# Kernel optimization log

Measured on AMD Instinct MI355X. Metric: run time of the kernel, lower is better.

Reference implementation:

```python
import jax, jax.numpy as jnp
import numpy as np
import math

B, H, S, DK = 4, 16, 2048, 64

def setup_inputs() -> dict:
    key = jax.random.key(0)
    kq, kk, kv, km = jax.random.split(key, 4)
    Q = jax.random.normal(kq, (B, H, S, DK), dtype=jnp.float32)
    K = jax.random.normal(kk, (B, H, S, DK), dtype=jnp.float32)
    V = jax.random.normal(kv, (B, H, S, DK), dtype=jnp.float32)
    # boolean mask [B, Sq, Sk]; True positions are masked out (set to -1e9)
    mask = jax.random.randint(km, (B, S, S), 0, 2).astype(jnp.bool_)
    return {"Q": Q, "K": K, "V": V, "mask": mask}

def reference(Q, K, V, mask):
    d_k = Q.shape[-1]
    # [B,H,Sq,Sk] scores
    scores = jnp.einsum('bhqd,bhkd->bhqk', Q, K) / math.sqrt(d_k)
    # mask [B,Sq,Sk] broadcasts over head dim (torch code repeats over heads)
    scores = jnp.where(mask[:, None, :, :], jnp.float32(-1e9), scores)
    attn = jax.nn.softmax(scores, axis=-1)
    out = jnp.einsum('bhqk,bhkd->bhqd', attn, V)
    return (out, attn)
```

## Files before the change

### kernel.cpp

```cpp
#include <hip/hip_runtime.h>
#include <cstdint>
#include <cstddef>

#define S_LEN 2048
#define DKD   64
#define BQ    64
#define BK    128
#define NKT   16
#define BDIM  256

typedef float f32x4 __attribute__((ext_vector_type(4)));
typedef short s16x8 __attribute__((ext_vector_type(8)));
typedef short s16x4 __attribute__((ext_vector_type(4)));
typedef unsigned short u16t;
typedef unsigned long long u64t;

#define KS_OFF    0
#define KT_BYTES  (BK * DKD * 2)
#define VT_OFF    16384
#define VT_BYTES  (DKD * BK * 2)
#define PS_OFF    32768
#define PS_STRIDE 264
#define SMEM_SZ   (PS_OFF + BQ * PS_STRIDE)

__device__ __forceinline__ u16t f2bf(float f) {
  unsigned u = __builtin_bit_cast(unsigned, f);
  return (u16t)((u + 0x7FFFu + ((u >> 16) & 1u)) >> 16);
}
__device__ __forceinline__ float bf_lo(unsigned u) {
  return __builtin_bit_cast(float, u << 16);
}
__device__ __forceinline__ float bf_hi(unsigned u) {
  return __builtin_bit_cast(float, u & 0xFFFF0000u);
}

__device__ __forceinline__ void gl_lds16(const void* g, void* l) {
  typedef __attribute__((address_space(1))) void gvoid;
  typedef __attribute__((address_space(3))) void lvoid;
  __builtin_amdgcn_global_load_lds((gvoid*)(void*)g, (lvoid*)l, 16, 0, 0);
}

#define BAR_VM(N) do { asm volatile("s_waitcnt vmcnt(" #N ")\n\ts_barrier" ::: "memory"); \
                       __builtin_amdgcn_sched_barrier(0); } while (0)
#define BAR_LGKM() do { asm volatile("s_waitcnt lgkmcnt(0)\n\ts_barrier" ::: "memory"); \
                        __builtin_amdgcn_sched_barrier(0); } while (0)

__global__ __launch_bounds__(256)
void prologue(const unsigned char* __restrict__ Mg, const float* __restrict__ Kg,
              const float* __restrict__ Vg, u64t* __restrict__ bits,
              u16t* __restrict__ Kws, u16t* __restrict__ Vws) {
  __shared__ float scr[BK][DKD + 1];
  __shared__ int mflag_s;
  const int tid = threadIdx.x;
  const int bid = blockIdx.x;

  if (bid < 1024) {
    int f = 0;
    for (int i = tid; i < 4096; i += 256) if ((i & 3) && Mg[i]) f = 1;
    if (tid == 0) mflag_s = 0;
    __syncthreads();
    if (f) mflag_s = 1;
    __syncthreads();
    const int mstride = mflag_s ? 1 : 4;

    const int row = bid * 8 + (tid >> 5);
    const int wd  = tid & 31;
    const size_t kbase = (size_t)row * S_LEN + (size_t)wd * 64;
    u64t word = 0;
    if (mstride == 1) {
      const u64t* p = (const u64t*)(Mg + kbase);
      #pragma unroll
      for (int i = 0; i < 8; ++i) {
        u64t x = p[i];
        u64t nz = x | (x >> 4); nz |= nz >> 2; nz |= nz >> 1;
        nz &= 0x0101010101010101ull;
        word |= ((nz * 0x0102040810204080ull) >> 56) << (8 * i);
      }
    } else {
      const unsigned* p = (const unsigned*)Mg + kbase;
      #pragma unroll
      for (int i = 0; i < 64; ++i) word |= (u64t)(p[i] ? 1u : 0u) << i;
    }
    bits[(size_t)row * 32 + wd] = word;
  } else if (bid < 2048) {
    const int kb = bid - 1024;
    const float* src = Kg + (size_t)kb * (BK * DKD);
    u16t* dst = Kws + (size_t)kb * (BK * DKD);
    #pragma unroll
    for (int i = 0; i < 4; ++i) {
      int c = tid + 256 * i;
      int row = c >> 3, y = c & 7;
      int oc = y ^ (row & 7);
      const float4* s4 = (const float4*)(src + row * DKD + 8 * oc);
      float4 a = s4[0], b = s4[1];
      s16x8 h = { (short)f2bf(a.x), (short)f2bf(a.y), (short)f2bf(a.z), (short)f2bf(a.w),
                  (short)f2bf(b.x), (short)f2bf(b.y), (short)f2bf(b.z), (short)f2bf(b.w) };
      *(s16x8*)(dst + row * DKD + 8 * y) = h;
    }
  } else {
    const int vb = bid - 2048;
    const float4* src = (const float4*)(Vg + (size_t)vb * (BK * DKD));
    #pragma unroll
    for (int i = 0; i < 8; ++i) {
      int c = tid + 256 * i;
      float4 v = src[c];
      int k = c >> 4, d0 = (c & 15) * 4;
      scr[k][d0] = v.x; scr[k][d0 + 1] = v.y; scr[k][d0 + 2] = v.z; scr[k][d0 + 3] = v.w;
    }
    __syncthreads();
    u16t* dst = Vws + (size_t)vb * (DKD * BK);
    #pragma unroll
    for (int i = 0; i < 8; ++i) {
      int c = tid + 256 * i;
      int dv = c >> 5, y = c & 31;
      int k0 = 4 * (y ^ (dv & 7));
      ushort4 h = make_ushort4(f2bf(scr[k0][dv]), f2bf(scr[k0 + 1][dv]),
                               f2bf(scr[k0 + 2][dv]), f2bf(scr[k0 + 3][dv]));
      *(ushort4*)(dst + dv * BK + 4 * y) = h;
    }
  }
}

__global__ __launch_bounds__(256)
void attn_ws(const float* __restrict__ Qg, const u16t* __restrict__ Kws,
             const u16t* __restrict__ Vws, const u64t* __restrict__ bits,
             float* __restrict__ outg, float* __restrict__ attng) {
  __shared__ char smem[SMEM_SZ];
  const int tid = threadIdx.x;
  const int p = blockIdx.x;
  const int qb = (p >> 3) & 31;
  const int bh = (p & 7) + 8 * (p >> 8);
  const int b  = bh >> 4;
  const int lane = tid & 63, wv = tid >> 6;
  const int cl = lane & 15, g = lane >> 4;
  const int q0 = qb * BQ + 16 * wv + 4 * g;
  const int swzK = (cl & 7) << 4;
  const int swzV = (cl & 7) << 3;

  const char* Kbh = (const char*)Kws + (size_t)bh * NKT * KT_BYTES;
  const char* Vbh = (const char*)Vws + (size_t)bh * NKT * VT_BYTES;

  float* oRow[4]; const u64t* bitRow[4];
  #pragma unroll
  for (int r = 0; r < 4; ++r) {
    oRow[r] = outg + (size_t)(bh * S_LEN + q0 + r) * DKD + cl;
    bitRow[r] = bits + (size_t)(b * S_LEN + q0 + r) * 32;
  }
  float* attnQ = attng + ((size_t)bh * S_LEN + (size_t)qb * BQ) * S_LEN;

  s16x8 aq0, aq1;
  {
    const float* qrow = Qg + ((size_t)bh * S_LEN + qb * BQ + 16 * wv + cl) * DKD;
    float x[8], y[8];
    *(float4*)(x)     = *(const float4*)(qrow + 8 * g);
    *(float4*)(x + 4) = *(const float4*)(qrow + 8 * g + 4);
    *(float4*)(y)     = *(const float4*)(qrow + 32 + 8 * g);
    *(float4*)(y + 4) = *(const float4*)(qrow + 32 + 8 * g + 4);
    #pragma unroll
    for (int j = 0; j < 8; ++j) { aq0[j] = (short)f2bf(x[j]); aq1[j] = (short)f2bf(y[j]); }
  }

  auto stageK = [&](int kt, int off) {
    const char* src = Kbh + (size_t)kt * KT_BYTES + wv * 4096 + lane * 16;
    #pragma unroll
    for (int t = 0; t < 4; ++t)
      gl_lds16(src + t * 1024, (void*)(smem + off + wv * 4096 + t * 1024));
  };
  auto stageV = [&](int kt) {
    const char* src = Vbh + (size_t)kt * VT_BYTES + wv * 4096 + lane * 16;
    #pragma unroll
    for (int t = 0; t < 4; ++t)
      gl_lds16(src + t * 1024, (void*)(smem + VT_OFF + wv * 4096 + t * 1024));
  };

  float lsum[4] = {0.f, 0.f, 0.f, 0.f};
  stageK(0, KS_OFF);
  for (int kt = 0; kt < NKT; ++kt) {
    const int cur = (kt & 1) ? VT_OFF : KS_OFF;
    if (kt + 1 < NKT) {
      stageK(kt + 1, (kt & 1) ? KS_OFF : VT_OFF);
      BAR_VM(4);
    } else {
      BAR_VM(0);
    }
    f32x4 accs[8];
    #pragma unroll
    for (int s = 0; s < 8; ++s) {
      const char* rb = smem + cur + (16 * s + cl) * 128;
      s16x8 b0 = *(const s16x8*)(rb + ((16 * g) ^ swzK));
      s16x8 b1 = *(const s16x8*)(rb + ((64 + 16 * g) ^ swzK));
      f32x4 acc = {0.f, 0.f, 0.f, 0.f};
      acc = __builtin_amdgcn_mfma_f32_16x16x32_bf16(aq0, b0, acc, 0, 0, 0);
      acc = __builtin_amdgcn_mfma_f32_16x16x32_bf16(aq1, b1, acc, 0, 0, 0);
      accs[s] = acc;
    }
    u64t bw0[4], bw1[4];
    #pragma unroll
    for (int r = 0; r < 4; ++r) { bw0[r] = bitRow[r][2 * kt]; bw1[r] = bitRow[r][2 * kt + 1]; }
    #pragma unroll
    for (int r = 0; r < 4; ++r) {
      float sum = 0.f;
      #pragma unroll
      for (int s = 0; s < 8; ++s) {
        bool mk = (((s < 4) ? bw0[r] : bw1[r]) >> ((16 * s + cl) & 63)) & 1ull;
        float e = __expf(accs[s][r] * 0.125f);
        sum += mk ? 0.f : e;
      }
      lsum[r] += sum;
    }
    BAR_LGKM();
  }
  float rinv[4];
  #pragma unroll
  for (int r = 0; r < 4; ++r) {
    float l = lsum[r];
    #pragma unroll
    for (int d = 1; d < 16; d <<= 1) l += __shfl_xor(l, d);
    rinv[r] = 1.f / l;
  }

  f32x4 accpv[4];
  #pragma unroll
  for (int db = 0; db < 4; ++db) accpv[db] = (f32x4){0.f, 0.f, 0.f, 0.f};

  stageK(0, KS_OFF);
  stageV(0);
  for (int kt = 0; kt < NKT; ++kt) {
    __syncthreads();
    u64t bw0[4], bw1[4];
    #pragma unroll
    for (int r = 0; r < 4; ++r) { bw0[r] = bitRow[r][2 * kt]; bw1[r] = bitRow[r][2 * kt + 1]; }

    #pragma unroll
    for (int ks = 0; ks < 4; ++ks) {
      f32x4 qa[2];
      #pragma unroll
      for (int sp = 0; sp < 2; ++sp) {
        int s = 2 * ks + sp;
        const char* rb = smem + KS_OFF + (16 * s + cl) * 128;
        s16x8 b0 = *(const s16x8*)(rb + ((16 * g) ^ swzK));
        s16x8 b1 = *(const s16x8*)(rb + ((64 + 16 * g) ^ swzK));
        f32x4 acc = {0.f, 0.f, 0.f, 0.f};
        acc = __builtin_amdgcn_mfma_f32_16x16x32_bf16(aq0, b0, acc, 0, 0, 0);
        acc = __builtin_amdgcn_mfma_f32_16x16x32_bf16(aq1, b1, acc, 0, 0, 0);
        qa[sp] = acc;
      }
      #pragma unroll
      for (int sp = 0; sp < 2; ++sp) {
        int s = 2 * ks + sp;
        #pragma unroll
        for (int r = 0; r < 4; ++r) {
          bool mk = (((s < 4) ? bw0[r] : bw1[r]) >> ((16 * s + cl) & 63)) & 1ull;
          float pv = mk ? 0.f : __expf(qa[sp][r] * 0.125f) * rinv[r];
          *(u16t*)(smem + PS_OFF + (16 * wv + 4 * g + r) * PS_STRIDE +
                   (32 * ks + 16 * sp + cl) * 2) = f2bf(pv);
        }
      }
      s16x4 p0 = *(const s16x4*)(smem + PS_OFF + (16 * wv + cl) * PS_STRIDE + (32 * ks + 4 * g) * 2);
      s16x4 p1 = *(const s16x4*)(smem + PS_OFF + (16 * wv + cl) * PS_STRIDE + (32 * ks + 16 + 4 * g) * 2);
      s16x8 pa = __builtin_shufflevector(p0, p1, 0, 1, 2, 3, 4, 5, 6, 7);
      #pragma unroll
      for (int db = 0; db < 4; ++db) {
        const char* vrow = smem + VT_OFF + (16 * db + cl) * 256;
        s16x4 v0 = *(const s16x4*)(vrow + ((64 * ks + 8 * g) ^ swzV));
        s16x4 v1 = *(const s16x4*)(vrow + ((64 * ks + 32 + 8 * g) ^ swzV));
        s16x8 vb = __builtin_shufflevector(v0, v1, 0, 1, 2, 3, 4, 5, 6, 7);
        accpv[db] = __builtin_amdgcn_mfma_f32_16x16x32_bf16(pa, vb, accpv[db], 0, 0, 0);
      }
    }
    __syncthreads();

    if (kt + 1 < NKT) { stageK(kt + 1, KS_OFF); stageV(kt + 1); }

    #pragma unroll
    for (int i = 0; i < 4; ++i) {
      int c = tid + 256 * i;
      int q = c >> 4, ch = c & 15;
      uint4 d = *(const uint4*)(smem + PS_OFF + q * PS_STRIDE + ch * 16);
      f32x4 lo = { bf_lo(d.x), bf_hi(d.x), bf_lo(d.y), bf_hi(d.y) };
      f32x4 hi = { bf_lo(d.z), bf_hi(d.z), bf_lo(d.w), bf_hi(d.w) };
      float* dst = attnQ + (size_t)q * S_LEN + kt * BK + ch * 8;
      __builtin_nontemporal_store(lo, (f32x4*)dst);
      __builtin_nontemporal_store(hi, (f32x4*)(dst + 4));
    }
  }

  #pragma unroll
  for (int db = 0; db < 4; ++db)
    #pragma unroll
    for (int r = 0; r < 4; ++r)
      oRow[r][16 * db] = accpv[db][r];
}

#define FB_KSTR 144
#define FB_VOFF (BK * FB_KSTR)
#define FB_VSTR 272
#define FB_POFF (FB_VOFF + DKD * FB_VSTR)
#define FB_SMEM (FB_POFF + BQ * FB_VSTR)

__global__ __launch_bounds__(256)
void attn_fb(const float* __restrict__ Qg, const float* __restrict__ Kg,
             const float* __restrict__ Vg, const unsigned char* __restrict__ Mg,
             float* __restrict__ outg, float* __restrict__ attng) {
  __shared__ char smem[FB_SMEM];
  __shared__ int mflag_s;
  const int tid = threadIdx.x;
  const int p = blockIdx.x;
  const int qb = (p >> 3) & 31;
  const int bh = (p & 7) + 8 * (p >> 8);
  const int b  = bh >> 4;

  int f = 0;
  for (int i = tid; i < 4096; i += BDIM) if ((i & 3) && Mg[i]) f = 1;
  if (tid == 0) mflag_s = 0;
  __syncthreads();
  if (f) mflag_s = 1;
  __syncthreads();
  const int mstride = mflag_s ? 1 : 4;

  const int lane = tid & 63, wv = tid >> 6;
  const int cl = lane & 15, g = lane >> 4;
  const int q0 = qb * BQ + 16 * wv + 4 * g;

  const float* Kbh = Kg + (size_t)bh * S_LEN * DKD;
  const float* Vbh = Vg + (size_t)bh * S_LEN * DKD;

  float* aRow[4]; float* oRow[4]; const unsigned char* mRow[4];
  #pragma unroll
  for (int r = 0; r < 4; ++r) {
    aRow[r] = attng + (size_t)(bh * S_LEN + q0 + r) * S_LEN + cl;
    oRow[r] = outg + (size_t)(bh * S_LEN + q0 + r) * DKD + cl;
    mRow[r] = Mg + ((size_t)(b * S_LEN + q0 + r) * S_LEN + cl) * (size_t)mstride;
  }

  s16x8 aq0, aq1;
  {
    const float* qrow = Qg + ((size_t)bh * S_LEN + qb * BQ + 16 * wv + cl) * DKD;
    float x[8], y[8];
    *(float4*)(x)     = *(const float4*)(qrow + 8 * g);
    *(float4*)(x + 4) = *(const float4*)(qrow + 8 * g + 4);
    *(float4*)(y)     = *(const float4*)(qrow + 32 + 8 * g);
    *(float4*)(y + 4) = *(const float4*)(qrow + 32 + 8 * g + 4);
    #pragma unroll
    for (int j = 0; j < 8; ++j) { aq0[j] = (short)f2bf(x[j]); aq1[j] = (short)f2bf(y[j]); }
  }

  float lsum[4] = {0.f, 0.f, 0.f, 0.f};
  for (int kt = 0; kt < NKT; ++kt) {
    const float4* ksrc = (const float4*)(Kbh + (size_t)kt * (BK * DKD));
    #pragma unroll
    for (int it = 0; it < 8; ++it) {
      int c = tid + BDIM * it;
      float4 v = ksrc[c];
      *(ushort4*)(smem + (c >> 4) * FB_KSTR + (c & 15) * 8) =
          make_ushort4(f2bf(v.x), f2bf(v.y), f2bf(v.z), f2bf(v.w));
    }
    __syncthreads();
    #pragma unroll
    for (int s = 0; s < 8; ++s) {
      s16x8 b0 = *(const s16x8*)(smem + (16 * s + cl) * FB_KSTR + 16 * g);
      s16x8 b1 = *(const s16x8*)(smem + (16 * s + cl) * FB_KSTR + 64 + 16 * g);
      f32x4 acc = {0.f, 0.f, 0.f, 0.f};
      acc = __builtin_amdgcn_mfma_f32_16x16x32_bf16(aq0, b0, acc, 0, 0, 0);
      acc = __builtin_amdgcn_mfma_f32_16x16x32_bf16(aq1, b1, acc, 0, 0, 0);
      #pragma unroll
      for (int r = 0; r < 4; ++r) {
        bool mk = mRow[r][(size_t)(kt * BK + 16 * s) * mstride] != 0;
        lsum[r] += mk ? 0.f : __expf(acc[r] * 0.125f);
      }
    }
    __syncthreads();
  }
  float rinv[4];
  #pragma unroll
  for (int r = 0; r < 4; ++r) {
    float l = lsum[r];
    #pragma unroll
    for (int d = 1; d < 16; d <<= 1) l += __shfl_xor(l, d);
    rinv[r] = 1.f / l;
  }

  f32x4 accpv[4];
  #pragma unroll
  for (int db = 0; db < 4; ++db) accpv[db] = (f32x4){0.f, 0.f, 0.f, 0.f};

  for (int kt = 0; kt < NKT; ++kt) {
    const float4* ksrc = (const float4*)(Kbh + (size_t)kt * (BK * DKD));
    #pragma unroll
    for (int it = 0; it < 8; ++it) {
      int c = tid + BDIM * it;
      float4 v = ksrc[c];
      *(ushort4*)(smem + (c >> 4) * FB_KSTR + (c & 15) * 8) =
          make_ushort4(f2bf(v.x), f2bf(v.y), f2bf(v.z), f2bf(v.w));
    }
    const float4* vsrc = (const float4*)(Vbh + (size_t)kt * (BK * DKD));
    #pragma unroll
    for (int it = 0; it < 8; ++it) {
      int c = tid + BDIM * it;
      float4 v = vsrc[c];
      int k = c >> 4, d0 = (c & 15) * 4;
      *(u16t*)(smem + FB_VOFF + (d0 + 0) * FB_VSTR + k * 2) = f2bf(v.x);
      *(u16t*)(smem + FB_VOFF + (d0 + 1) * FB_VSTR + k * 2) = f2bf(v.y);
      *(u16t*)(smem + FB_VOFF + (d0 + 2) * FB_VSTR + k * 2) = f2bf(v.z);
      *(u16t*)(smem + FB_VOFF + (d0 + 3) * FB_VSTR + k * 2) = f2bf(v.w);
    }
    __syncthreads();

    #pragma unroll
    for (int ks = 0; ks < 4; ++ks) {
      f32x4 qa[2];
      #pragma unroll
      for (int sp = 0; sp < 2; ++sp) {
        int s = 2 * ks + sp;
        s16x8 b0 = *(const s16x8*)(smem + (16 * s + cl) * FB_KSTR + 16 * g);
        s16x8 b1 = *(const s16x8*)(smem + (16 * s + cl) * FB_KSTR + 64 + 16 * g);
        f32x4 acc = {0.f, 0.f, 0.f, 0.f};
        acc = __builtin_amdgcn_mfma_f32_16x16x32_bf16(aq0, b0, acc, 0, 0, 0);
        acc = __builtin_amdgcn_mfma_f32_16x16x32_bf16(aq1, b1, acc, 0, 0, 0);
        qa[sp] = acc;
      }
      #pragma unroll
      for (int sp = 0; sp < 2; ++sp) {
        int s = 2 * ks + sp;
        #pragma unroll
        for (int r = 0; r < 4; ++r) {
          bool mk = mRow[r][(size_t)(kt * BK + 16 * s) * mstride] != 0;
          float pv = mk ? 0.f : __expf(qa[sp][r] * 0.125f) * rinv[r];
          __builtin_nontemporal_store(pv, aRow[r] + kt * BK + 16 * s);
          *(u16t*)(smem + FB_POFF + (16 * wv + 4 * g + r) * FB_VSTR +
                   (32 * ks + 16 * sp + cl) * 2) = f2bf(pv);
        }
      }
      s16x4 p0 = *(const s16x4*)(smem + FB_POFF + (16 * wv + cl) * FB_VSTR + (32 * ks + 4 * g) * 2);
      s16x4 p1 = *(const s16x4*)(smem + FB_POFF + (16 * wv + cl) * FB_VSTR + (32 * ks + 16 + 4 * g) * 2);
      s16x8 pa = __builtin_shufflevector(p0, p1, 0, 1, 2, 3, 4, 5, 6, 7);
      #pragma unroll
      for (int db = 0; db < 4; ++db) {
        s16x4 v0 = *(const s16x4*)(smem + FB_VOFF + (16 * db + cl) * FB_VSTR + (32 * ks + 4 * g) * 2);
        s16x4 v1 = *(const s16x4*)(smem + FB_VOFF + (16 * db + cl) * FB_VSTR + (32 * ks + 16 + 4 * g) * 2);
        s16x8 vb = __builtin_shufflevector(v0, v1, 0, 1, 2, 3, 4, 5, 6, 7);
        accpv[db] = __builtin_amdgcn_mfma_f32_16x16x32_bf16(pa, vb, accpv[db], 0, 0, 0);
      }
    }
    __syncthreads();
  }

  #pragma unroll
  for (int db = 0; db < 4; ++db)
    #pragma unroll
    for (int r = 0; r < 4; ++r)
      oRow[r][16 * db] = accpv[db][r];
}

extern "C" void kernel_launch(void* const* d_in, const int* in_sizes, int n_in,
                              void* d_out, int out_size, void* d_ws, size_t ws_size,
                              hipStream_t stream) {
  const float* Q = (const float*)d_in[0];
  const float* K = (const float*)d_in[1];
  const float* V = (const float*)d_in[2];
  const unsigned char* M = (const unsigned char*)d_in[3];
  float* out = (float*)d_out;
  float* attn = out + (size_t)4 * 16 * S_LEN * DKD;

  const size_t BITS_SZ = (size_t)4 * S_LEN * 32 * 8;
  const size_t KWS_SZ  = (size_t)64 * NKT * BK * DKD * 2;
  const size_t VWS_SZ  = (size_t)64 * NKT * DKD * BK * 2;
  if (ws_size >= BITS_SZ + KWS_SZ + VWS_SZ) {
    u64t* bits = (u64t*)d_ws;
    u16t* Kws = (u16t*)((char*)d_ws + BITS_SZ);
    u16t* Vws = (u16t*)((char*)d_ws + BITS_SZ + KWS_SZ);
    prologue<<<3072, 256, 0, stream>>>(M, K, V, bits, Kws, Vws);
    attn_ws<<<2048, BDIM, 0, stream>>>(Q, Kws, Vws, bits, out, attn);
  } else {
    attn_fb<<<2048, BDIM, 0, stream>>>(Q, K, V, M, out, attn);
  }
}
```

Before: 367.5 us.

## Transpose score MFMA so P stays in registers and simplify mask handling

The QK^T MFMA operands are swapped so each lane holds scores for a single query row. This lets the softmax denominator use one accumulator with two cross-lane shuffles, lets the mask be read as one 16-byte load per tile, and lets P be packed straight into the PV MFMA operand without an LDS write-then-read round trip. P is still written to LDS, with a new padded stride, for the attn output store. Full __syncthreads barriers are replaced with explicit waitcnt barriers that allow the attn stores to overlap the next tile's loads. The barrier choice (vmcnt(8) at the end of the loop) is fragile and could race if the count of outstanding memory ops changes.

```diff
diff --git a/kernel.cpp b/kernel.cpp
--- a/kernel.cpp
+++ b/kernel.cpp
@@ -12,6 +12,7 @@
 typedef float f32x4 __attribute__((ext_vector_type(4)));
 typedef short s16x8 __attribute__((ext_vector_type(8)));
 typedef short s16x4 __attribute__((ext_vector_type(4)));
+typedef unsigned int u32x4 __attribute__((ext_vector_type(4)));
 typedef unsigned short u16t;
 typedef unsigned long long u64t;
 
@@ -20,7 +21,7 @@
 #define VT_OFF    16384
 #define VT_BYTES  (DKD * BK * 2)
 #define PS_OFF    32768
-#define PS_STRIDE 264
+#define PS_STRIDE 280
 #define SMEM_SZ   (PS_OFF + BQ * PS_STRIDE)
 
 __device__ __forceinline__ u16t f2bf(float f) {
@@ -42,8 +43,10 @@
 
 #define BAR_VM(N) do { asm volatile("s_waitcnt vmcnt(" #N ")\n\ts_barrier" ::: "memory"); \
                        __builtin_amdgcn_sched_barrier(0); } while (0)
-#define BAR_LGKM() do { asm volatile("s_waitcnt lgkmcnt(0)\n\ts_barrier" ::: "memory"); \
-                        __builtin_amdgcn_sched_barrier(0); } while (0)
+#define BAR_LG()  do { asm volatile("s_waitcnt lgkmcnt(0)\n\ts_barrier" ::: "memory"); \
+                       __builtin_amdgcn_sched_barrier(0); } while (0)
+#define BAR_VM8() do { asm volatile("s_waitcnt vmcnt(8) lgkmcnt(0)\n\ts_barrier" ::: "memory"); \
+                       __builtin_amdgcn_sched_barrier(0); } while (0)
 
 __global__ __launch_bounds__(256)
 void prologue(const unsigned char* __restrict__ Mg, const float* __restrict__ Kg,
@@ -133,29 +136,28 @@
   const int b  = bh >> 4;
   const int lane = tid & 63, wv = tid >> 6;
   const int cl = lane & 15, g = lane >> 4;
-  const int q0 = qb * BQ + 16 * wv + 4 * g;
+  const int qrow = qb * BQ + 16 * wv + cl;
   const int swzK = (cl & 7) << 4;
   const int swzV = (cl & 7) << 3;
 
   const char* Kbh = (const char*)Kws + (size_t)bh * NKT * KT_BYTES;
   const char* Vbh = (const char*)Vws + (size_t)bh * NKT * VT_BYTES;
-
-  float* oRow[4]; const u64t* bitRow[4];
-  #pragma unroll
-  for (int r = 0; r < 4; ++r) {
-    oRow[r] = outg + (size_t)(bh * S_LEN + q0 + r) * DKD + cl;
-    bitRow[r] = bits + (size_t)(b * S_LEN + q0 + r) * 32;
-  }
+  const u64t* bitR = bits + (size_t)(b * S_LEN + qrow) * 32;
   float* attnQ = attng + ((size_t)bh * S_LEN + (size_t)qb * BQ) * S_LEN;
+
+  float* oRow[4];
+  #pragma unroll
+  for (int r = 0; r < 4; ++r)
+    oRow[r] = outg + (size_t)(bh * S_LEN + qb * BQ + 16 * wv + 4 * g + r) * DKD + cl;
 
   s16x8 aq0, aq1;
   {
-    const float* qrow = Qg + ((size_t)bh * S_LEN + qb * BQ + 16 * wv + cl) * DKD;
+    const float* qr = Qg + ((size_t)bh * S_LEN + qrow) * DKD;
     float x[8], y[8];
-    *(float4*)(x)     = *(const float4*)(qrow + 8 * g);
-    *(float4*)(x + 4) = *(const float4*)(qrow + 8 * g + 4);
-    *(float4*)(y)     = *(const float4*)(qrow + 32 + 8 * g);
-    *(float4*)(y + 4) = *(const float4*)(qrow + 32 + 8 * g + 4);
+    *(float4*)(x)     = *(const float4*)(qr + 8 * g);
+    *(float4*)(x + 4) = *(const float4*)(qr + 8 * g + 4);
+    *(float4*)(y)     = *(const float4*)(qr + 32 + 8 * g);
+    *(float4*)(y + 4) = *(const float4*)(qr + 32 + 8 * g + 4);
     #pragma unroll
     for (int j = 0; j < 8; ++j) { aq0[j] = (short)f2bf(x[j]); aq1[j] = (short)f2bf(y[j]); }
   }
@@ -173,7 +175,7 @@
       gl_lds16(src + t * 1024, (void*)(smem + VT_OFF + wv * 4096 + t * 1024));
   };
 
-  float lsum[4] = {0.f, 0.f, 0.f, 0.f};
+  float lsum = 0.f;
   stageK(0, KS_OFF);
   for (int kt = 0; kt < NKT; ++kt) {
     const int cur = (kt & 1) ? VT_OFF : KS_OFF;
@@ -183,41 +185,25 @@
     } else {
       BAR_VM(0);
     }
-    f32x4 accs[8];
+    ulonglong2 bw = *(const ulonglong2*)(bitR + 2 * kt);
     #pragma unroll
     for (int s = 0; s < 8; ++s) {
       const char* rb = smem + cur + (16 * s + cl) * 128;
-      s16x8 b0 = *(const s16x8*)(rb + ((16 * g) ^ swzK));
-      s16x8 b1 = *(const s16x8*)(rb + ((64 + 16 * g) ^ swzK));
+      s16x8 k0 = *(const s16x8*)(rb + ((16 * g) ^ swzK));
+      s16x8 k1 = *(const s16x8*)(rb + ((64 + 16 * g) ^ swzK));
       f32x4 acc = {0.f, 0.f, 0.f, 0.f};
-      acc = __builtin_amdgcn_mfma_f32_16x16x32_bf16(aq0, b0, acc, 0, 0, 0);
-      acc = __builtin_amdgcn_mfma_f32_16x16x32_bf16(aq1, b1, acc, 0, 0, 0);
-      accs[s] = acc;
-    }
-    u64t bw0[4], bw1[4];
-    #pragma unroll
-    for (int r = 0; r < 4; ++r) { bw0[r] = bitRow[r][2 * kt]; bw1[r] = bitRow[r][2 * kt + 1]; }
-    #pragma unroll
-    for (int r = 0; r < 4; ++r) {
-      float sum = 0.f;
-      #pragma unroll
-      for (int s = 0; s < 8; ++s) {
-        bool mk = (((s < 4) ? bw0[r] : bw1[r]) >> ((16 * s + cl) & 63)) & 1ull;
-        float e = __expf(accs[s][r] * 0.125f);
-        sum += mk ? 0.f : e;
-      }
-      lsum[r] += sum;
-    }
-    BAR_LGKM();
-  }
-  float rinv[4];
-  #pragma unroll
-  for (int r = 0; r < 4; ++r) {
-    float l = lsum[r];
-    #pragma unroll
-    for (int d = 1; d < 16; d <<= 1) l += __shfl_xor(l, d);
-    rinv[r] = 1.f / l;
-  }
+      acc = __builtin_amdgcn_mfma_f32_16x16x32_bf16(k0, aq0, acc, 0, 0, 0);
+      acc = __builtin_amdgcn_mfma_f32_16x16x32_bf16(k1, aq1, acc, 0, 0, 0);
+      unsigned nib = (unsigned)(((s < 4) ? bw.x : bw.y) >> (16 * (s & 3) + 4 * g)) & 0xFu;
+      #pragma unroll
+      for (int r = 0; r < 4; ++r)
+        lsum += ((nib >> r) & 1) ? 0.f : __expf(acc[r] * 0.125f);
+    }
+    BAR_LG();
+  }
+  lsum += __shfl_xor(lsum, 16);
+  lsum += __shfl_xor(lsum, 32);
+  const float rinv = 1.f / lsum;
 
   f32x4 accpv[4];
   #pragma unroll
@@ -225,11 +211,10 @@
 
   stageK(0, KS_OFF);
   stageV(0);
+  BAR_VM(0);
   for (int kt = 0; kt < NKT; ++kt) {
-    __syncthreads();
-    u64t bw0[4], bw1[4];
-    #pragma unroll
-    for (int r = 0; r < 4; ++r) { bw0[r] = bitRow[r][2 * kt]; bw1[r] = bitRow[r][2 * kt + 1]; }
+    ulonglong2 bw = *(const ulonglong2*)(bitR + 2 * kt);
+    char* pbase = smem + PS_OFF + (16 * wv + cl) * PS_STRIDE;
 
     #pragma unroll
     for (int ks = 0; ks < 4; ++ks) {
@@ -238,27 +223,28 @@
       for (int sp = 0; sp < 2; ++sp) {
         int s = 2 * ks + sp;
         const char* rb = smem + KS_OFF + (16 * s + cl) * 128;
-        s16x8 b0 = *(const s16x8*)(rb + ((16 * g) ^ swzK));
-        s16x8 b1 = *(const s16x8*)(rb + ((64 + 16 * g) ^ swzK));
+        s16x8 k0 = *(const s16x8*)(rb + ((16 * g) ^ swzK));
+        s16x8 k1 = *(const s16x8*)(rb + ((64 + 16 * g) ^ swzK));
         f32x4 acc = {0.f, 0.f, 0.f, 0.f};
-        acc = __builtin_amdgcn_mfma_f32_16x16x32_bf16(aq0, b0, acc, 0, 0, 0);
-        acc = __builtin_amdgcn_mfma_f32_16x16x32_bf16(aq1, b1, acc, 0, 0, 0);
+        acc = __builtin_amdgcn_mfma_f32_16x16x32_bf16(k0, aq0, acc, 0, 0, 0);
+        acc = __builtin_amdgcn_mfma_f32_16x16x32_bf16(k1, aq1, acc, 0, 0, 0);
         qa[sp] = acc;
       }
+      unsigned hw[4];
       #pragma unroll
       for (int sp = 0; sp < 2; ++sp) {
         int s = 2 * ks + sp;
+        unsigned nib = (unsigned)(((s < 4) ? bw.x : bw.y) >> (16 * (s & 3) + 4 * g)) & 0xFu;
         #pragma unroll
-        for (int r = 0; r < 4; ++r) {
-          bool mk = (((s < 4) ? bw0[r] : bw1[r]) >> ((16 * s + cl) & 63)) & 1ull;
-          float pv = mk ? 0.f : __expf(qa[sp][r] * 0.125f) * rinv[r];
-          *(u16t*)(smem + PS_OFF + (16 * wv + 4 * g + r) * PS_STRIDE +
-                   (32 * ks + 16 * sp + cl) * 2) = f2bf(pv);
+        for (int rr = 0; rr < 2; ++rr) {
+          float p0 = ((nib >> (2 * rr)) & 1)     ? 0.f : __expf(qa[sp][2 * rr] * 0.125f) * rinv;
+          float p1 = ((nib >> (2 * rr + 1)) & 1) ? 0.f : __expf(qa[sp][2 * rr + 1] * 0.125f) * rinv;
+          hw[2 * sp + rr] = (unsigned)f2bf(p0) | ((unsigned)f2bf(p1) << 16);
         }
       }
-      s16x4 p0 = *(const s16x4*)(smem + PS_OFF + (16 * wv + cl) * PS_STRIDE + (32 * ks + 4 * g) * 2);
-      s16x4 p1 = *(const s16x4*)(smem + PS_OFF + (16 * wv + cl) * PS_STRIDE + (32 * ks + 16 + 4 * g) * 2);
-      s16x8 pa = __builtin_shufflevector(p0, p1, 0, 1, 2, 3, 4, 5, 6, 7);
+      *(uint2*)(pbase + 64 * ks + 8 * g)      = make_uint2(hw[0], hw[1]);
+      *(uint2*)(pbase + 64 * ks + 32 + 8 * g) = make_uint2(hw[2], hw[3]);
+      s16x8 pa = __builtin_bit_cast(s16x8, (u32x4){hw[0], hw[1], hw[2], hw[3]});
       #pragma unroll
       for (int db = 0; db < 4; ++db) {
         const char* vrow = smem + VT_OFF + (16 * db + cl) * 256;
@@ -268,7 +254,8 @@
         accpv[db] = __builtin_amdgcn_mfma_f32_16x16x32_bf16(pa, vb, accpv[db], 0, 0, 0);
       }
     }
-    __syncthreads();
+
+    BAR_LG();
 
     if (kt + 1 < NKT) { stageK(kt + 1, KS_OFF); stageV(kt + 1); }
 
@@ -276,13 +263,15 @@
     for (int i = 0; i < 4; ++i) {
       int c = tid + 256 * i;
       int q = c >> 4, ch = c & 15;
-      uint4 d = *(const uint4*)(smem + PS_OFF + q * PS_STRIDE + ch * 16);
+      u32x4 d = *(const u32x4*)(smem + PS_OFF + q * PS_STRIDE + ch * 16);
       f32x4 lo = { bf_lo(d.x), bf_hi(d.x), bf_lo(d.y), bf_hi(d.y) };
       f32x4 hi = { bf_lo(d.z), bf_hi(d.z), bf_lo(d.w), bf_hi(d.w) };
       float* dst = attnQ + (size_t)q * S_LEN + kt * BK + ch * 8;
       __builtin_nontemporal_store(lo, (f32x4*)dst);
       __builtin_nontemporal_store(hi, (f32x4*)(dst + 4));
     }
+
+    if (kt + 1 < NKT) BAR_VM8();
   }
 
   #pragma unroll
```

Measured after the change: 348.5 us. 5.2% less time.
